# Performance work log

Measured on AMD Instinct MI355X. Metric: run time of the kernel, lower is better.

The kernel has to match this reference:

```python
import jax, jax.numpy as jnp
import numpy as np

N_EMBD = 1024
N_HEAD = 16
HORIZON = 64
HS = N_EMBD // N_HEAD        # 64
BD = max(HS // 4, 16)        # 16


def setup_inputs() -> dict:
    key = jax.random.key(0)
    ks = jax.random.split(key, 12)
    s = 0.02
    B, T = 2, 1024
    return {
        "x": jax.random.normal(ks[0], (B, T, N_EMBD), jnp.float32),
        "W_disp": jax.random.normal(ks[1], (N_EMBD, N_HEAD * BD), jnp.float32) * s,
        "W_val": jax.random.normal(ks[2], (N_EMBD, N_EMBD), jnp.float32) * s,
        "rel_pos_emb": jax.random.normal(ks[3], (HORIZON, BD), jnp.float32) * s,
        "W_strain": jax.random.normal(ks[4], (BD, BD), jnp.float32) * s,
        "W_pos": jax.random.normal(ks[5], (BD, BD), jnp.float32) * s,
        "W_bond": jax.random.normal(ks[6], (BD, 1), jnp.float32) * s,
        "W_dmg": jax.random.normal(ks[7], (BD, BD), jnp.float32) * s,
        "b_dmg": jnp.zeros((BD,), jnp.float32),
        "W_dmg_out": jax.random.normal(ks[8], (BD, 1), jnp.float32) * s,
        "b_dmg_out": jnp.full((1,), -3.0, jnp.float32),  # nn.init.constant_(damage_out.bias, -3.0)
        "W_cproj": jax.random.normal(ks[9], (N_EMBD, N_EMBD), jnp.float32) * s,
    }


def _windows(t, delta):
    # t: (B, nh, T, D) -> (B, nh, T, delta, D); causal sliding window via left pad
    B, nh, T, D = t.shape
    padded = jnp.pad(t, ((0, 0), (0, 0), (delta - 1, 0), (0, 0)))
    idx = jnp.arange(T)[:, None] + jnp.arange(delta)[None, :]  # (T, delta)
    return padded[:, :, idx]  # gather over time axis


def reference(x, W_disp, W_val, rel_pos_emb, W_strain, W_pos, W_bond,
              W_dmg, b_dmg, W_dmg_out, b_dmg_out, W_cproj):
    B, T, C = x.shape
    nh, bd, hs = N_HEAD, BD, HS
    delta = min(HORIZON, T)

    disp = (x @ W_disp).reshape(B, T, nh, bd).transpose(0, 2, 1, 3)  # (B,nh,T,bd)
    val = (x @ W_val).reshape(B, T, nh, hs).transpose(0, 2, 1, 3)    # (B,nh,T,hs)

    disp_win = _windows(disp, delta)  # (B,nh,T,delta,bd)
    val_win = _windows(val, delta)    # (B,nh,T,delta,hs)

    # causal mask: window slot w for token t maps to position t - delta + 1 + w
    cmask = (jnp.arange(T)[:, None] - delta + 1 + jnp.arange(delta)[None, :]) >= 0  # (T,delta)

    strain = disp_win - disp[:, :, :, None, :]  # (B,nh,T,delta,bd)
    rel_emb = rel_pos_emb[:delta]               # (delta,bd)

    bond_act = jax.nn.gelu(strain @ W_strain + rel_emb @ W_pos, approximate=False)
    bond_logits = (bond_act @ W_bond)[..., 0]   # (B,nh,T,delta)

    damage_act = jax.nn.gelu(strain @ W_dmg + b_dmg, approximate=False)
    damage = jax.nn.sigmoid((damage_act @ W_dmg_out)[..., 0] + b_dmg_out[0])

    logits = bond_logits - 10.0 * damage
    logits = jnp.where(cmask[None, None], logits, -jnp.inf)
    weights = jax.nn.softmax(logits, axis=-1)

    out = jnp.einsum('bntd,bntde->bnte', weights, val_win)  # (B,nh,T,hs)
    out = out.transpose(0, 2, 1, 3).reshape(B, T, C)
    return out @ W_cproj
```

## Files before the change

### kernel.cpp

```cpp
#include <hip/hip_runtime.h>
#include <hip/hip_bf16.h>
#include <hip/hip_fp16.h>
#include <math.h>

#define TB   2
#define TT   1024
#define TC   1024
#define NH   16
#define HS   64
#define BDI  16
#define DLT  64
#define GK   1024
#define NDV  1280

typedef __attribute__((ext_vector_type(8))) short short8;
typedef __attribute__((ext_vector_type(4))) float floatx4;
typedef __attribute__((ext_vector_type(16))) float floatx16;
typedef __hip_bfloat16 bf16;

__device__ __forceinline__ unsigned pkbf(float a, float b) {
    return (__float_as_uint(a) >> 16) | (__float_as_uint(b) & 0xFFFF0000u);
}

__device__ __forceinline__ unsigned bfbits(float x) {
    bf16 h = __float2bfloat16(x);
    return (unsigned)*(unsigned short*)&h;
}

__device__ __forceinline__ __half2 gelu_pk(__half2 x, __half2 kc1, __half2 kc2,
                                           __half2 khalf) {
    __half2 y = __hmul2(x, x);
    __half2 p = __hfma2(y, kc2, kc1);
    return __hfma2(x, khalf, __hmul2(y, p));
}

__device__ __forceinline__ void gload_lds16(const void* g, void* l) {
    __builtin_amdgcn_global_load_lds(
        (const __attribute__((address_space(1))) unsigned int*)(unsigned long long)g,
        (__attribute__((address_space(3))) unsigned int*)(unsigned int)(unsigned long long)l,
        16, 0, 0);
}

__device__ __forceinline__ void tpose_body(const float* __restrict__ in,
                                           bf16* __restrict__ outp,
                                           int k0, int n0, int N,
                                           float (*tile)[33], int tid) {
    const int tx = tid & 31, ty4 = (tid >> 5) * 4;
#pragma unroll
    for (int i = 0; i < 4; i++)
        tile[ty4 + i][tx] = in[(long long)(k0 + ty4 + i) * N + n0 + tx];
    __syncthreads();
#pragma unroll
    for (int i = 0; i < 4; i++)
        outp[(long long)(n0 + ty4 + i) * TC + k0 + tx] = __float2bfloat16(tile[tx][ty4 + i]);
}

__global__ __launch_bounds__(256) void prep_k(
    const float* __restrict__ x, const float* __restrict__ Wdisp,
    const float* __restrict__ Wval, const float* __restrict__ Wc,
    const float* __restrict__ rel, const float* __restrict__ Wp,
    bf16* __restrict__ xb, bf16* __restrict__ Wdvt, bf16* __restrict__ Wct,
    float* __restrict__ peG) {
    __shared__ float tile[32][33];
    const int blk = blockIdx.x, tid = threadIdx.x;
    if (blk < 2048) {
        int i = blk * 1024 + tid * 4;
        float4 v = *(const float4*)(x + i);
        bf16 o0 = __float2bfloat16(v.x), o1 = __float2bfloat16(v.y);
        bf16 o2 = __float2bfloat16(v.z), o3 = __float2bfloat16(v.w);
        ushort4 u;
        u.x = *(unsigned short*)&o0; u.y = *(unsigned short*)&o1;
        u.z = *(unsigned short*)&o2; u.w = *(unsigned short*)&o3;
        *(ushort4*)(xb + i) = u;
    } else if (blk < 2304) {
        int l = blk - 2048;
        tpose_body(Wdisp, Wdvt, (l >> 3) * 32, (l & 7) * 32, 256, tile, tid);
    } else if (blk < 3328) {
        int l = blk - 2304;
        tpose_body(Wval, Wdvt + (size_t)256 * TC, (l >> 5) * 32, (l & 31) * 32, TC, tile, tid);
    } else if (blk < 4352) {
        int l = blk - 3328;
        tpose_body(Wc, Wct, (l >> 5) * 32, (l & 31) * 32, TC, tile, tid);
    } else {
        int idx = (blk - 4352) * 256 + tid;
        int j = idx >> 4, d = idx & 15;
        float s = 0.f;
#pragma unroll
        for (int k = 0; k < BDI; k++)
            s += rel[j * BDI + k] * Wp[k * BDI + d];
        peG[idx] = s;
    }
}

template <int ID>
__global__ __launch_bounds__(256) void mfma_gemm_k(const bf16* __restrict__ A,
                                                   const bf16* __restrict__ Bt,
                                                   float* __restrict__ C,
                                                   bf16* __restrict__ valT,
                                                   int M, int N, int nbx) {
    __shared__ __align__(16) bf16 As[2][64 * 128];
    __shared__ __align__(16) bf16 Bs[2][64 * 128];
    const int tid = threadIdx.x;
    const int w = tid >> 6, lane = tid & 63;

    const int xcd = blockIdx.x & 7, s0 = blockIdx.x >> 3;
    const int l = xcd * (gridDim.x >> 3) + s0;
    const int row0 = (l / nbx) * 64, col0 = (l % nbx) * 64;
    const int wm = (w >> 1) * 32, wn = (w & 1) * 32;

    const bf16* gA[4];
    const bf16* gB[4];
    int lofs[4];
#pragma unroll
    for (int p = 0; p < 4; p++) {
        int u = (p * 4 + w) * 64 + lane;
        int r = u >> 4, s = u & 15;
        int c = s ^ (r & 15);
        gA[p] = A  + (long long)(row0 + r) * GK + c * 8;
        gB[p] = Bt + (long long)(col0 + r) * GK + c * 8;
        lofs[p] = (p * 4 + w) * 512;
    }

    floatx4 acc[2][2] = {};
    const int rA = lane & 15, quad = lane >> 4;

#pragma unroll
    for (int p = 0; p < 4; p++) {
        gload_lds16(gA[p], &As[0][lofs[p]]);
        gload_lds16(gB[p], &Bs[0][lofs[p]]);
    }

    int cur = 0;
    for (int k0 = 0; k0 < GK; k0 += 128) {
        __syncthreads();
        if (k0 + 128 < GK) {
#pragma unroll
            for (int p = 0; p < 4; p++) {
                gload_lds16(gA[p] + k0 + 128, &As[cur ^ 1][lofs[p]]);
                gload_lds16(gB[p] + k0 + 128, &Bs[cur ^ 1][lofs[p]]);
            }
        }
        const bf16* Ac = As[cur];
        const bf16* Bc = Bs[cur];
#pragma unroll
        for (int kh = 0; kh < 4; kh++) {
            const int g = kh * 4 + quad;
            short8 af[2], bfr[2];
#pragma unroll
            for (int i = 0; i < 2; i++) {
                af[i]  = *(const short8*)&Ac[(wm + i * 16 + rA) * 128 + ((g ^ rA) * 8)];
                bfr[i] = *(const short8*)&Bc[(wn + i * 16 + rA) * 128 + ((g ^ rA) * 8)];
            }
#pragma unroll
            for (int i = 0; i < 2; i++)
#pragma unroll
                for (int j = 0; j < 2; j++)
                    acc[i][j] = __builtin_amdgcn_mfma_f32_16x16x32_bf16(af[i], bfr[j], acc[i][j], 0, 0, 0);
        }
        cur ^= 1;
    }
    const int cn = lane & 15, rq = (lane >> 4) * 4;
    if (ID == 1 && col0 >= 256) {
        __syncthreads();
        unsigned short (*eT)[68] = (unsigned short (*)[68])As;
#pragma unroll
        for (int i = 0; i < 2; i++)
#pragma unroll
            for (int j = 0; j < 2; j++) {
                int e = wn + j * 16 + cn;
                int t = wm + i * 16 + rq;
                uint2 st;
                st.x = bfbits(acc[i][j][0]) | (bfbits(acc[i][j][1]) << 16);
                st.y = bfbits(acc[i][j][2]) | (bfbits(acc[i][j][3]) << 16);
                *(uint2*)&eT[e][t] = st;
            }
        __syncthreads();
        const int hh = (col0 - 256) >> 6;
        const int bb = row0 >> 10;
        const int trow0 = row0 & (TT - 1);
        bf16* base = valT + (size_t)((bb * NH + hh) * HS) * TT + trow0;
        for (int idx = tid; idx < 512; idx += 256) {
            int e = idx >> 3, c = idx & 7;
            *(uint4*)(base + (size_t)e * TT + c * 8) = *(const uint4*)&eT[e][c * 8];
        }
    } else {
#pragma unroll
        for (int i = 0; i < 2; i++)
#pragma unroll
            for (int j = 0; j < 2; j++) {
                long long base = (long long)(row0 + wm + i * 16 + rq) * N + col0 + wn + j * 16 + cn;
#pragma unroll
                for (int r = 0; r < 4; r++)
                    C[base + (long long)r * N] = acc[i][j][r];
            }
    }
}

__global__ __launch_bounds__(256, 8) void attn_k(
    const float* __restrict__ dispC,
    const bf16* __restrict__ valT,
    const float* __restrict__ peG,
    const float* __restrict__ W_strain,
    const float* __restrict__ W_dmg,
    const float* __restrict__ W_bond,
    const float* __restrict__ b_dmg,
    const float* __restrict__ W_dmg_out,
    const float* __restrict__ b_dmg_out,
    bf16* __restrict__ attnout) {
    __shared__ __align__(16) float          sDisp[79][20];
    __shared__ __align__(16) unsigned short sWgtS[16][104];
    __shared__ __align__(16) __half2        sPE[64][12];

    const int tid = threadIdx.x;
    const int wave = tid >> 6, lane = tid & 63;
    const int xcd = blockIdx.x & 7, slot = blockIdx.x >> 3;
    const int bh = xcd * 4 + (slot >> 6);
    const int t0 = (slot & 63) * 16;
    const int h = bh & (NH - 1);
    const int b = bh >> 4;

    if (tid < 208) ((int4*)sWgtS)[tid] = make_int4(0, 0, 0, 0);

    for (int idx = tid; idx < 79 * 4; idx += 256) {
        int r = idx >> 2, c = idx & 3;
        int row = t0 - 63 + r; row = row < 0 ? 0 : row;
        *(float4*)&sDisp[r][c * 4] =
            *(const float4*)(dispC + (long long)(b * TT + row) * 256 + h * BDI + c * 4);
    }
    for (int idx = tid; idx < 512; idx += 256) {
        int j = idx >> 3, dp = idx & 7;
        sPE[j][dp] = __floats2half2_rn(peG[j * BDI + 2 * dp], peG[j * BDI + 2 * dp + 1]);
    }

    const int n = lane & 31, hi = lane >> 5;
    union U8 { short8 s8; unsigned u[4]; };
    const floatx16 z16 = {};

    short8 aw;
    {
        const float* wsel = (n < 16) ? (W_strain + n) : (W_dmg + (n - 16));
        float wv[8];
#pragma unroll
        for (int e = 0; e < 8; e++) wv[e] = wsel[(8 * hi + e) * BDI];
        U8 a;
#pragma unroll
        for (int q = 0; q < 4; q++) a.u[q] = pkbf(wv[2 * q], wv[2 * q + 1]);
        aw = a.s8;
    }
    __half2 pbd[4], wbp[4], wdp[4];
    {
        float4 bdA = *(const float4*)(b_dmg + 4 * hi);
        float4 bdB = *(const float4*)(b_dmg + 8 + 4 * hi);
        pbd[0] = __floats2half2_rn(bdA.x, bdA.y); pbd[1] = __floats2half2_rn(bdA.z, bdA.w);
        pbd[2] = __floats2half2_rn(bdB.x, bdB.y); pbd[3] = __floats2half2_rn(bdB.z, bdB.w);
        float4 wbA = *(const float4*)(W_bond + 4 * hi);
        float4 wbB = *(const float4*)(W_bond + 8 + 4 * hi);
        float4 wdA = *(const float4*)(W_dmg_out + 4 * hi);
        float4 wdB = *(const float4*)(W_dmg_out + 8 + 4 * hi);
        wbp[0] = __floats2half2_rn(wbA.x, wbA.y); wbp[1] = __floats2half2_rn(wbA.z, wbA.w);
        wbp[2] = __floats2half2_rn(wbB.x, wbB.y); wbp[3] = __floats2half2_rn(wbB.z, wbB.w);
        wdp[0] = __floats2half2_rn(wdA.x, wdA.y); wdp[1] = __floats2half2_rn(wdA.z, wdA.w);
        wdp[2] = __floats2half2_rn(wdB.x, wdB.y); wdp[3] = __floats2half2_rn(wdB.z, wdB.w);
    }
    const float bdo0 = b_dmg_out[0];
    const __half2 kc1   = __floats2half2_rn(0.3989422804f, 0.3989422804f);
    const __half2 kc2   = __floats2half2_rn(-0.06649038006f, -0.06649038006f);
    const __half2 khalf = __floats2half2_rn(0.5f, 0.5f);

    __syncthreads();

#pragma unroll
    for (int s = 0; s < 4; s++) {
        const int tau = 4 * wave + s;
        float oc[8];
        {
            const float* op = &sDisp[tau + 63][8 * hi];
            *(float4*)&oc[0] = *(const float4*)op;
            *(float4*)&oc[4] = *(const float4*)(op + 4);
        }
        float ee[2];
#pragma unroll
        for (int h2 = 0; h2 < 2; h2++) {
            const int j = 32 * h2 + n;
            const float* rp = &sDisp[tau + j][8 * hi];
            float p[8];
            *(float4*)&p[0] = *(const float4*)rp;
            *(float4*)&p[4] = *(const float4*)(rp + 4);
            U8 t_;
#pragma unroll
            for (int pp = 0; pp < 4; pp++)
                t_.u[pp] = pkbf(p[2 * pp] - oc[2 * pp], p[2 * pp + 1] - oc[2 * pp + 1]);
            floatx16 c2 = __builtin_amdgcn_mfma_f32_32x32x16_bf16(aw, t_.s8, z16, 0, 0, 0);
            uint2 pA = *(const uint2*)&sPE[j][2 * hi];
            uint2 pB = *(const uint2*)&sPE[j][4 + 2 * hi];
            __half2 pbb[4];
            pbb[0] = *(__half2*)&pA.x; pbb[1] = *(__half2*)&pA.y;
            pbb[2] = *(__half2*)&pB.x; pbb[3] = *(__half2*)&pB.y;
            __half2 accb = __floats2half2_rn(0.f, 0.f);
            __half2 accd = __floats2half2_rn(0.f, 0.f);
#pragma unroll
            for (int i = 0; i < 4; i++) {
                __half2 xb_ = __hadd2(__floats2half2_rn(c2[2 * i], c2[2 * i + 1]), pbb[i]);
                __half2 xd_ = __hadd2(__floats2half2_rn(c2[8 + 2 * i], c2[9 + 2 * i]), pbd[i]);
                accb = __hfma2(gelu_pk(xb_, kc1, kc2, khalf), wbp[i], accb);
                accd = __hfma2(gelu_pk(xd_, kc1, kc2, khalf), wdp[i], accd);
            }
            float bond = __low2float(accb) + __high2float(accb);
            float dmgv = __low2float(accd) + __high2float(accd);
            bond += __shfl_xor(bond, 32);
            dmgv += __shfl_xor(dmgv, 32);
            float damage = 1.f / (1.f + __expf(-(dmgv + bdo0)));
            const bool valid = (t0 + tau + j - 63) >= 0;
            ee[h2] = valid ? __expf(bond - 10.f * damage) : 0.f;
        }
        float sm = ee[0] + ee[1];
#pragma unroll
        for (int off = 16; off >= 1; off >>= 1) sm += __shfl_xor(sm, off);
        float inv = 1.0f / sm;
        if (hi == 0) {
            sWgtS[tau][tau + 1 + n]  = (unsigned short)bfbits(ee[0] * inv);
            sWgtS[tau][tau + 33 + n] = (unsigned short)bfbits(ee[1] * inv);
        }
    }
    __syncthreads();

    const int m = lane & 15, quad = lane >> 4;
    const floatx4 zf = {0.f, 0.f, 0.f, 0.f};
    const bf16* vbase = valT + ((size_t)(b * NH + h) * HS + 16 * wave + m) * TT;
    floatx4 acc = zf;
#pragma unroll
    for (int c = 0; c < 3; c++) {
        int toff = t0 - 64 + c * 32 + quad * 8;
        toff = toff < 0 ? 0 : (toff > TT - 8 ? TT - 8 : toff);
        short8 afr = *(const short8*)&sWgtS[m][c * 32 + quad * 8];
        short8 bfr = *(const short8*)(vbase + toff);
        acc = __builtin_amdgcn_mfma_f32_16x16x32_bf16(afr, bfr, acc, 0, 0, 0);
    }
    const int e0 = 16 * wave + m;
#pragma unroll
    for (int r = 0; r < 4; r++) {
        int tau = quad * 4 + r;
        attnout[(long long)(b * TT + t0 + tau) * TC + h * HS + e0] = __float2bfloat16(acc[r]);
    }
}

extern "C" void kernel_launch(void* const* d_in, const int* in_sizes, int n_in,
                              void* d_out, int out_size, void* d_ws, size_t ws_size,
                              hipStream_t stream) {
    const float* x      = (const float*)d_in[0];
    const float* W_disp = (const float*)d_in[1];
    const float* W_val  = (const float*)d_in[2];
    const float* rel    = (const float*)d_in[3];
    const float* Ws     = (const float*)d_in[4];
    const float* Wp     = (const float*)d_in[5];
    const float* Wb     = (const float*)d_in[6];
    const float* Wd     = (const float*)d_in[7];
    const float* bd_    = (const float*)d_in[8];
    const float* Wdo    = (const float*)d_in[9];
    const float* bdo    = (const float*)d_in[10];
    const float* Wc     = (const float*)d_in[11];
    float* out = (float*)d_out;

    const int M = TB * TT;
    char* ws = (char*)d_ws;
    bf16*  xb    = (bf16*)ws;
    bf16*  attnb = (bf16*)ws;
    bf16*  Wdvt  = (bf16*)(ws + (size_t)4 * 1024 * 1024);
    bf16*  Wct   = (bf16*)(ws + (size_t)6656 * 1024);
    float* dispC = (float*)(ws + (size_t)8704 * 1024);
    bf16*  valT  = (bf16*)(ws + (size_t)10752 * 1024);
    float* peG   = (float*)(ws + (size_t)14848 * 1024);

    dim3 blk(256);
    prep_k<<<4356, blk, 0, stream>>>(x, W_disp, W_val, Wc, rel, Wp,
                                     xb, Wdvt, Wct, peG);
    mfma_gemm_k<1><<<(M / 64) * (NDV / 64), blk, 0, stream>>>(xb, Wdvt, dispC, valT, M, 256, NDV / 64);
    attn_k<<<(TB * NH * TT) / 16, blk, 0, stream>>>(dispC, valT, peG, Ws, Wd, Wb, bd_,
                                                    Wdo, bdo, attnb);
    mfma_gemm_k<2><<<(M / 64) * (TC / 64), blk, 0, stream>>>(attnb, Wct, out, nullptr, M, TC, TC / 64);
}
```

Measured before the change: 129.5 us.

## Fold strain/damage projections into disp GEMM weights and simplify attention scoring

Because strain is linear in disp, the kernel precomputes W_disp_h·W_strain and W_disp_h·W_dmg per head in the prep kernel. The first GEMM then emits projected P/Q values directly, packed as fp16 pairs in a time-padded transposed layout. The attention kernel no longer builds bf16 strain tiles or runs a 32x32 MFMA per window slot. Each lane now does half2 subtract, GELU and dot work over 16 dims, using async global-to-LDS loads. The price is a wider first GEMM (1280 to 1536 columns) and more fp16 rounding on the projected values.

```diff
diff --git a/kernel.cpp b/kernel.cpp
--- a/kernel.cpp
+++ b/kernel.cpp
@@ -11,20 +11,24 @@
 #define BDI  16
 #define DLT  64
 #define GK   1024
-#define NDV  1280
+#define NDV  1536
+#define PQS  1152
 
 typedef __attribute__((ext_vector_type(8))) short short8;
 typedef __attribute__((ext_vector_type(4))) float floatx4;
-typedef __attribute__((ext_vector_type(16))) float floatx16;
 typedef __hip_bfloat16 bf16;
-
-__device__ __forceinline__ unsigned pkbf(float a, float b) {
-    return (__float_as_uint(a) >> 16) | (__float_as_uint(b) & 0xFFFF0000u);
-}
 
 __device__ __forceinline__ unsigned bfbits(float x) {
     bf16 h = __float2bfloat16(x);
     return (unsigned)*(unsigned short*)&h;
+}
+__device__ __forceinline__ unsigned short hfbits(float x) {
+    __half h = __float2half_rn(x);
+    return *(unsigned short*)&h;
+}
+__device__ __forceinline__ unsigned packh2(float lo, float hi) {
+    __half2 h = __floats2half2_rn(lo, hi);
+    return *(unsigned*)&h;
 }
 
 __device__ __forceinline__ __half2 gelu_pk(__half2 x, __half2 kc1, __half2 kc2,
@@ -59,6 +63,7 @@
     const float* __restrict__ x, const float* __restrict__ Wdisp,
     const float* __restrict__ Wval, const float* __restrict__ Wc,
     const float* __restrict__ rel, const float* __restrict__ Wp,
+    const float* __restrict__ Ws, const float* __restrict__ Wd,
     bf16* __restrict__ xb, bf16* __restrict__ Wdvt, bf16* __restrict__ Wct,
     float* __restrict__ peG) {
     __shared__ float tile[32][33];
@@ -66,23 +71,29 @@
     if (blk < 2048) {
         int i = blk * 1024 + tid * 4;
         float4 v = *(const float4*)(x + i);
-        bf16 o0 = __float2bfloat16(v.x), o1 = __float2bfloat16(v.y);
-        bf16 o2 = __float2bfloat16(v.z), o3 = __float2bfloat16(v.w);
         ushort4 u;
-        u.x = *(unsigned short*)&o0; u.y = *(unsigned short*)&o1;
-        u.z = *(unsigned short*)&o2; u.w = *(unsigned short*)&o3;
+        u.x = (unsigned short)bfbits(v.x); u.y = (unsigned short)bfbits(v.y);
+        u.z = (unsigned short)bfbits(v.z); u.w = (unsigned short)bfbits(v.w);
         *(ushort4*)(xb + i) = u;
-    } else if (blk < 2304) {
-        int l = blk - 2048;
-        tpose_body(Wdisp, Wdvt, (l >> 3) * 32, (l & 7) * 32, 256, tile, tid);
-    } else if (blk < 3328) {
-        int l = blk - 2304;
-        tpose_body(Wval, Wdvt + (size_t)256 * TC, (l >> 5) * 32, (l & 31) * 32, TC, tile, tid);
-    } else if (blk < 4352) {
-        int l = blk - 3328;
+    } else if (blk < 4096) {
+        int idx = (blk - 2048) * 256 + tid;
+        int k = idx & 1023, n = idx >> 10;
+        int h = n >> 5, pq = (n >> 4) & 1, d2 = n & 15;
+        const float* Wsel = pq ? Wd : Ws;
+        const float* wrow = Wdisp + (size_t)k * 256 + h * 16;
+        float s = 0.f;
+#pragma unroll
+        for (int d = 0; d < BDI; d++)
+            s = fmaf(wrow[d], Wsel[d * BDI + d2], s);
+        Wdvt[(size_t)n * TC + k] = __float2bfloat16(s);
+    } else if (blk < 5120) {
+        int l = blk - 4096;
+        tpose_body(Wval, Wdvt + (size_t)512 * TC, (l >> 5) * 32, (l & 31) * 32, TC, tile, tid);
+    } else if (blk < 6144) {
+        int l = blk - 5120;
         tpose_body(Wc, Wct, (l >> 5) * 32, (l & 31) * 32, TC, tile, tid);
     } else {
-        int idx = (blk - 4352) * 256 + tid;
+        int idx = (blk - 6144) * 256 + tid;
         int j = idx >> 4, d = idx & 15;
         float s = 0.f;
 #pragma unroll
@@ -97,6 +108,7 @@
                                                    const bf16* __restrict__ Bt,
                                                    float* __restrict__ C,
                                                    bf16* __restrict__ valT,
+                                                   unsigned* __restrict__ pqT,
                                                    int M, int N, int nbx) {
     __shared__ __align__(16) bf16 As[2][64 * 128];
     __shared__ __align__(16) bf16 Bs[2][64 * 128];
@@ -160,7 +172,37 @@
         cur ^= 1;
     }
     const int cn = lane & 15, rq = (lane >> 4) * 4;
-    if (ID == 1 && col0 >= 256) {
+    if (ID == 1 && col0 < 512) {
+        __syncthreads();
+        unsigned short (*eT)[68] = (unsigned short (*)[68])As;
+#pragma unroll
+        for (int i = 0; i < 2; i++)
+#pragma unroll
+            for (int j = 0; j < 2; j++) {
+                int e = wn + j * 16 + cn;
+                int t = wm + i * 16 + rq;
+#pragma unroll
+                for (int r = 0; r < 4; r++)
+                    eT[e][t + r] = hfbits(acc[i][j][r]);
+            }
+        __syncthreads();
+        const int hbase = col0 >> 5;
+        const int bb = row0 >> 10, t0g = row0 & (TT - 1);
+        for (int idx = tid; idx < 512; idx += 256) {
+            int r = idx >> 4, c4 = idx & 15;
+            int hl = r >> 4, d2 = r & 15, tt = c4 * 4;
+            const unsigned short* pr = &eT[hl * 32 + d2][tt];
+            const unsigned short* qr = &eT[hl * 32 + 16 + d2][tt];
+            uint4 o;
+            o.x = (unsigned)pr[0] | ((unsigned)qr[0] << 16);
+            o.y = (unsigned)pr[1] | ((unsigned)qr[1] << 16);
+            o.z = (unsigned)pr[2] | ((unsigned)qr[2] << 16);
+            o.w = (unsigned)pr[3] | ((unsigned)qr[3] << 16);
+            unsigned* dst = pqT + (size_t)((bb * NH + hbase + hl) * BDI + d2) * PQS
+                          + 64 + t0g + tt;
+            *(uint4*)dst = o;
+        }
+    } else if (ID == 1) {
         __syncthreads();
         unsigned short (*eT)[68] = (unsigned short (*)[68])As;
 #pragma unroll
@@ -175,7 +217,7 @@
                 *(uint2*)&eT[e][t] = st;
             }
         __syncthreads();
-        const int hh = (col0 - 256) >> 6;
+        const int hh = (col0 - 512) >> 6;
         const int bb = row0 >> 10;
         const int trow0 = row0 & (TT - 1);
         bf16* base = valT + (size_t)((bb * NH + hh) * HS) * TT + trow0;
@@ -196,20 +238,18 @@
     }
 }
 
-__global__ __launch_bounds__(256, 8) void attn_k(
-    const float* __restrict__ dispC,
+__global__ __launch_bounds__(256) void attn_k(
+    const unsigned* __restrict__ pqT,
     const bf16* __restrict__ valT,
     const float* __restrict__ peG,
-    const float* __restrict__ W_strain,
-    const float* __restrict__ W_dmg,
+    const float* __restrict__ b_dmg,
     const float* __restrict__ W_bond,
-    const float* __restrict__ b_dmg,
     const float* __restrict__ W_dmg_out,
     const float* __restrict__ b_dmg_out,
     bf16* __restrict__ attnout) {
-    __shared__ __align__(16) float          sDisp[79][20];
+    __shared__ __align__(16) unsigned       sPQ[16][80];
+    __shared__ __align__(16) unsigned       sPEB[64][17];
     __shared__ __align__(16) unsigned short sWgtS[16][104];
-    __shared__ __align__(16) __half2        sPE[64][12];
 
     const int tid = threadIdx.x;
     const int wave = tid >> 6, lane = tid & 63;
@@ -219,48 +259,33 @@
     const int h = bh & (NH - 1);
     const int b = bh >> 4;
 
+    {
+        const unsigned* gbase = pqT + (size_t)(b * NH + h) * BDI * PQS + t0;
+        for (int task = tid; task < 320; task += 256) {
+            int d2 = task / 20, c = task - d2 * 20;
+            gload_lds16(gbase + (size_t)d2 * PQS + 4 * c,
+                        (char*)sPQ + (task & ~63) * 16);
+        }
+    }
     if (tid < 208) ((int4*)sWgtS)[tid] = make_int4(0, 0, 0, 0);
-
-    for (int idx = tid; idx < 79 * 4; idx += 256) {
-        int r = idx >> 2, c = idx & 3;
-        int row = t0 - 63 + r; row = row < 0 ? 0 : row;
-        *(float4*)&sDisp[r][c * 4] =
-            *(const float4*)(dispC + (long long)(b * TT + row) * 256 + h * BDI + c * 4);
-    }
-    for (int idx = tid; idx < 512; idx += 256) {
-        int j = idx >> 3, dp = idx & 7;
-        sPE[j][dp] = __floats2half2_rn(peG[j * BDI + 2 * dp], peG[j * BDI + 2 * dp + 1]);
-    }
-
-    const int n = lane & 31, hi = lane >> 5;
-    union U8 { short8 s8; unsigned u[4]; };
-    const floatx16 z16 = {};
-
-    short8 aw;
     {
-        const float* wsel = (n < 16) ? (W_strain + n) : (W_dmg + (n - 16));
-        float wv[8];
-#pragma unroll
-        for (int e = 0; e < 8; e++) wv[e] = wsel[(8 * hi + e) * BDI];
-        U8 a;
-#pragma unroll
-        for (int q = 0; q < 4; q++) a.u[q] = pkbf(wv[2 * q], wv[2 * q + 1]);
-        aw = a.s8;
-    }
-    __half2 pbd[4], wbp[4], wdp[4];
-    {
-        float4 bdA = *(const float4*)(b_dmg + 4 * hi);
-        float4 bdB = *(const float4*)(b_dmg + 8 + 4 * hi);
-        pbd[0] = __floats2half2_rn(bdA.x, bdA.y); pbd[1] = __floats2half2_rn(bdA.z, bdA.w);
-        pbd[2] = __floats2half2_rn(bdB.x, bdB.y); pbd[3] = __floats2half2_rn(bdB.z, bdB.w);
-        float4 wbA = *(const float4*)(W_bond + 4 * hi);
-        float4 wbB = *(const float4*)(W_bond + 8 + 4 * hi);
-        float4 wdA = *(const float4*)(W_dmg_out + 4 * hi);
-        float4 wdB = *(const float4*)(W_dmg_out + 8 + 4 * hi);
-        wbp[0] = __floats2half2_rn(wbA.x, wbA.y); wbp[1] = __floats2half2_rn(wbA.z, wbA.w);
-        wbp[2] = __floats2half2_rn(wbB.x, wbB.y); wbp[3] = __floats2half2_rn(wbB.z, wbB.w);
-        wdp[0] = __floats2half2_rn(wdA.x, wdA.y); wdp[1] = __floats2half2_rn(wdA.z, wdA.w);
-        wdp[2] = __floats2half2_rn(wdB.x, wdB.y); wdp[3] = __floats2half2_rn(wdB.z, wdB.w);
+        int j = tid >> 2, q4 = (tid & 3) * 4;
+        float4 pv = *(const float4*)(peG + j * BDI + q4);
+        float4 bv = *(const float4*)(b_dmg + q4);
+        sPEB[j][q4 + 0] = packh2(pv.x, bv.x);
+        sPEB[j][q4 + 1] = packh2(pv.y, bv.y);
+        sPEB[j][q4 + 2] = packh2(pv.z, bv.z);
+        sPEB[j][q4 + 3] = packh2(pv.w, bv.w);
+    }
+    __half2 w2[16];
+#pragma unroll
+    for (int q = 0; q < 4; q++) {
+        float4 wb = *(const float4*)(W_bond + 4 * q);
+        float4 wd = *(const float4*)(W_dmg_out + 4 * q);
+        w2[4 * q + 0] = __floats2half2_rn(wb.x, wd.x);
+        w2[4 * q + 1] = __floats2half2_rn(wb.y, wd.y);
+        w2[4 * q + 2] = __floats2half2_rn(wb.z, wd.z);
+        w2[4 * q + 3] = __floats2half2_rn(wb.w, wd.w);
     }
     const float bdo0 = b_dmg_out[0];
     const __half2 kc1   = __floats2half2_rn(0.3989422804f, 0.3989422804f);
@@ -269,58 +294,30 @@
 
     __syncthreads();
 
+    __half2 pb[16];
+#pragma unroll
+    for (int d2 = 0; d2 < 16; d2++) pb[d2] = *(const __half2*)&sPEB[lane][d2];
+
 #pragma unroll
     for (int s = 0; s < 4; s++) {
-        const int tau = 4 * wave + s;
-        float oc[8];
-        {
-            const float* op = &sDisp[tau + 63][8 * hi];
-            *(float4*)&oc[0] = *(const float4*)op;
-            *(float4*)&oc[4] = *(const float4*)(op + 4);
-        }
-        float ee[2];
-#pragma unroll
-        for (int h2 = 0; h2 < 2; h2++) {
-            const int j = 32 * h2 + n;
-            const float* rp = &sDisp[tau + j][8 * hi];
-            float p[8];
-            *(float4*)&p[0] = *(const float4*)rp;
-            *(float4*)&p[4] = *(const float4*)(rp + 4);
-            U8 t_;
-#pragma unroll
-            for (int pp = 0; pp < 4; pp++)
-                t_.u[pp] = pkbf(p[2 * pp] - oc[2 * pp], p[2 * pp + 1] - oc[2 * pp + 1]);
-            floatx16 c2 = __builtin_amdgcn_mfma_f32_32x32x16_bf16(aw, t_.s8, z16, 0, 0, 0);
-            uint2 pA = *(const uint2*)&sPE[j][2 * hi];
-            uint2 pB = *(const uint2*)&sPE[j][4 + 2 * hi];
-            __half2 pbb[4];
-            pbb[0] = *(__half2*)&pA.x; pbb[1] = *(__half2*)&pA.y;
-            pbb[2] = *(__half2*)&pB.x; pbb[3] = *(__half2*)&pB.y;
-            __half2 accb = __floats2half2_rn(0.f, 0.f);
-            __half2 accd = __floats2half2_rn(0.f, 0.f);
-#pragma unroll
-            for (int i = 0; i < 4; i++) {
-                __half2 xb_ = __hadd2(__floats2half2_rn(c2[2 * i], c2[2 * i + 1]), pbb[i]);
-                __half2 xd_ = __hadd2(__floats2half2_rn(c2[8 + 2 * i], c2[9 + 2 * i]), pbd[i]);
-                accb = __hfma2(gelu_pk(xb_, kc1, kc2, khalf), wbp[i], accb);
-                accd = __hfma2(gelu_pk(xd_, kc1, kc2, khalf), wdp[i], accd);
-            }
-            float bond = __low2float(accb) + __high2float(accb);
-            float dmgv = __low2float(accd) + __high2float(accd);
-            bond += __shfl_xor(bond, 32);
-            dmgv += __shfl_xor(dmgv, 32);
-            float damage = 1.f / (1.f + __expf(-(dmgv + bdo0)));
-            const bool valid = (t0 + tau + j - 63) >= 0;
-            ee[h2] = valid ? __expf(bond - 10.f * damage) : 0.f;
-        }
-        float sm = ee[0] + ee[1];
-#pragma unroll
-        for (int off = 16; off >= 1; off >>= 1) sm += __shfl_xor(sm, off);
-        float inv = 1.0f / sm;
-        if (hi == 0) {
-            sWgtS[tau][tau + 1 + n]  = (unsigned short)bfbits(ee[0] * inv);
-            sWgtS[tau][tau + 33 + n] = (unsigned short)bfbits(ee[1] * inv);
-        }
+        const int tl = 4 * wave + s;
+        __half2 acc = __floats2half2_rn(0.f, 0.f);
+#pragma unroll
+        for (int d2 = 0; d2 < 16; d2++) {
+            unsigned wv = sPQ[d2][tl + 1 + lane];
+            unsigned cv = sPQ[d2][tl + 64];
+            __half2 x = __hsub2(*(const __half2*)&wv, *(const __half2*)&cv);
+            x = __hadd2(x, pb[d2]);
+            acc = __hfma2(gelu_pk(x, kc1, kc2, khalf), w2[d2], acc);
+        }
+        float bond = __low2float(acc), dmgv = __high2float(acc);
+        float damage = 1.f / (1.f + __expf(-(dmgv + bdo0)));
+        const bool valid = (t0 + tl - 63 + lane) >= 0;
+        float e = valid ? __expf(bond - 10.f * damage) : 0.f;
+        float sm = e;
+#pragma unroll
+        for (int off = 32; off >= 1; off >>= 1) sm += __shfl_xor(sm, off);
+        sWgtS[tl][tl + 1 + lane] = (unsigned short)bfbits(e / sm);
     }
     __syncthreads();
 
@@ -363,19 +360,21 @@
 
     const int M = TB * TT;
     char* ws = (char*)d_ws;
-    bf16*  xb    = (bf16*)ws;
-    bf16*  attnb = (bf16*)ws;
-    bf16*  Wdvt  = (bf16*)(ws + (size_t)4 * 1024 * 1024);
-    bf16*  Wct   = (bf16*)(ws + (size_t)6656 * 1024);
-    float* dispC = (float*)(ws + (size_t)8704 * 1024);
-    bf16*  valT  = (bf16*)(ws + (size_t)10752 * 1024);
-    float* peG   = (float*)(ws + (size_t)14848 * 1024);
+    bf16*     xb    = (bf16*)ws;
+    bf16*     attnb = (bf16*)ws;
+    bf16*     Wdvt  = (bf16*)(ws + (size_t)4 * 1024 * 1024);
+    bf16*     Wct   = (bf16*)(ws + (size_t)7 * 1024 * 1024);
+    bf16*     valT  = (bf16*)(ws + (size_t)9 * 1024 * 1024);
+    unsigned* pqT   = (unsigned*)(ws + (size_t)13 * 1024 * 1024);
+    float*    peG   = (float*)(ws + (size_t)15872 * 1024);
 
     dim3 blk(256);
-    prep_k<<<4356, blk, 0, stream>>>(x, W_disp, W_val, Wc, rel, Wp,
+    prep_k<<<6148, blk, 0, stream>>>(x, W_disp, W_val, Wc, rel, Wp, Ws, Wd,
                                      xb, Wdvt, Wct, peG);
-    mfma_gemm_k<1><<<(M / 64) * (NDV / 64), blk, 0, stream>>>(xb, Wdvt, dispC, valT, M, 256, NDV / 64);
-    attn_k<<<(TB * NH * TT) / 16, blk, 0, stream>>>(dispC, valT, peG, Ws, Wd, Wb, bd_,
+    mfma_gemm_k<1><<<(M / 64) * (NDV / 64), blk, 0, stream>>>(xb, Wdvt, nullptr,
+                                                              valT, pqT, M, 0, NDV / 64);
+    attn_k<<<(TB * NH * TT) / 16, blk, 0, stream>>>(pqT, valT, peG, bd_, Wb,
                                                     Wdo, bdo, attnb);
-    mfma_gemm_k<2><<<(M / 64) * (TC / 64), blk, 0, stream>>>(attnb, Wct, out, nullptr, M, TC, TC / 64);
-}
+    mfma_gemm_k<2><<<(M / 64) * (TC / 64), blk, 0, stream>>>(attnb, Wct, out,
+                                                             nullptr, nullptr, M, TC, TC / 64);
+}
```

Result: no change. 127.2 us (-1.8%).
